# Performance work log

Measured on AMD Instinct MI355X. Metric: run time of the kernel, lower is better.

The kernel has to match this reference:

```python
import jax, jax.numpy as jnp
import numpy as np

B, S, D_IN, D_OUT, N, R = 8, 4096, 1280, 1280, 4, 16


def setup_inputs() -> dict:
    key = jax.random.key(0)
    ks = jax.random.split(key, 7)
    x = jax.random.normal(ks[0], (B, S, D_IN), dtype=jnp.float32)
    W = jax.random.normal(ks[1], (D_OUT, D_IN), dtype=jnp.float32) * 0.02
    bias = jax.random.normal(ks[2], (D_OUT,), dtype=jnp.float32) * 0.02
    A = jax.random.normal(ks[3], (N, R, D_IN), dtype=jnp.float32) * 0.02
    Bw = jax.random.normal(ks[4], (N, D_OUT, R), dtype=jnp.float32) * 0.02
    scalings = jax.random.uniform(ks[5], (N,), dtype=jnp.float32)
    masks = jax.random.uniform(ks[6], (N, S), dtype=jnp.float32)
    # normalize masks to sum ~1 per position, per docstring
    masks = masks / jnp.sum(masks, axis=0, keepdims=True)
    return {"x": x, "W": W, "bias": bias, "A": A, "Bw": Bw,
            "scalings": scalings, "masks": masks}


def reference(x, W, bias, A, Bw, scalings, masks):
    # base linear: y = x @ W^T + b
    base = jnp.einsum('bsd,od->bso', x, W) + bias
    # batched LoRA branches: h = x @ A_i^T  (b,s,n,r)
    h = jnp.einsum('bsd,nrd->bsnr', x, A)
    # lora_out_i = h @ B_i^T  (b,s,n,o)
    lora = jnp.einsum('bsnr,nor->bsno', h, Bw)
    # weighted sum over subjects: scaling_i * mask_i(pos)
    lora_sum = jnp.einsum('bsno,n,ns->bso', lora, scalings, masks)
    return base + lora_sum
```

## Files before the change

kernel.cpp:

```cpp
#include <hip/hip_runtime.h>
#include <hip/hip_bf16.h>
#include <stdint.h>

#define S_LEN   4096
#define DIN     1280
#define DOUT    1280
#define N_LORA  4
#define R_LORA  16
#define M_TOT   32768
#define KC      (DIN + N_LORA*R_LORA)

typedef __attribute__((ext_vector_type(4))) float floatx4;
typedef __attribute__((ext_vector_type(8))) short shortx8;

typedef union { uint4 u; shortx8 s; } punx8;

static __device__ __forceinline__ unsigned short bf16_rne(float f) {
    union { float f; unsigned u; } v; v.f = f;
    unsigned u = v.u;
    u += 0x7fffu + ((u >> 16) & 1u);
    return (unsigned short)(u >> 16);
}

static __device__ __forceinline__ void async16(const unsigned short* g, unsigned short* l) {
    __builtin_amdgcn_global_load_lds(
        (const __attribute__((address_space(1))) unsigned int*)g,
        (__attribute__((address_space(3))) unsigned int*)l, 16, 0, 0);
}

static __device__ __forceinline__ uint4 cvt8(const float* src) {
    const float4* p = (const float4*)src;
    float4 a = p[0], b = p[1];
    uint4 o;
    o.x = (unsigned)bf16_rne(a.x) | ((unsigned)bf16_rne(a.y) << 16);
    o.y = (unsigned)bf16_rne(a.z) | ((unsigned)bf16_rne(a.w) << 16);
    o.z = (unsigned)bf16_rne(b.x) | ((unsigned)bf16_rne(b.y) << 16);
    o.w = (unsigned)bf16_rne(b.z) | ((unsigned)bf16_rne(b.w) << 16);
    return o;
}

__global__ __launch_bounds__(256) void k_build_wcat(const float* __restrict__ W,
                                                    const float* __restrict__ Bw,
                                                    unsigned short* __restrict__ Wcat) {
    int i = blockIdx.x * 256 + threadIdx.x;
    int e = i * 8;
    int o = e / KC;
    int c = e - o * KC;
    const float* src;
    if (c < DIN) {
        src = W + o * DIN + c;
    } else {
        int j = c - DIN;
        int n = j >> 4, r = j & 15;
        src = Bw + (n * DOUT + o) * R_LORA + r;
    }
    *(uint4*)(Wcat + o * KC + c) = cvt8(src);
}

__global__ __launch_bounds__(256) void k_convert_a(const float* __restrict__ A,
                                                   unsigned short* __restrict__ Ab) {
    int i = blockIdx.x * 256 + threadIdx.x;
    int e = i * 8;
    *(uint4*)(Ab + e) = cvt8(A + e);
}

__global__ __launch_bounds__(256) void k_fused_x(const float* __restrict__ x,
                                                 const unsigned short* __restrict__ Ab,
                                                 const float* __restrict__ scalings,
                                                 const float* __restrict__ masks,
                                                 unsigned short* __restrict__ xg) {
    int tid = threadIdx.x;
    int wave = tid >> 6, lane = tid & 63;
    int mi = lane & 15, kq = lane >> 4;
    int m0 = blockIdx.x * 64;
    int m = m0 + wave * 16 + mi;

    const float* xrow = x + (size_t)m * DIN;
    unsigned short* xgrow = xg + (size_t)m * KC;

    floatx4 acc[4] = {};

    for (int k0 = 0; k0 < DIN; k0 += 32) {
        int k = k0 + kq * 8;
        punx8 xf; xf.u = cvt8(xrow + k);
        *(uint4*)(xgrow + k) = xf.u;
#pragma unroll
        for (int ct = 0; ct < 4; ++ct) {
            shortx8 bf = *(const shortx8*)(Ab + (ct * 16 + mi) * DIN + k);
            acc[ct] = __builtin_amdgcn_mfma_f32_16x16x32_bf16(xf.s, bf, acc[ct], 0, 0, 0);
        }
    }

#pragma unroll
    for (int ct = 0; ct < 4; ++ct) {
        float sc = scalings[ct];
        int j = ct * 16 + mi;
#pragma unroll
        for (int reg = 0; reg < 4; ++reg) {
            int m2 = m0 + wave * 16 + kq * 4 + reg;
            int s = m2 & (S_LEN - 1);
            float wgt = sc * masks[ct * S_LEN + s];
            xg[(size_t)m2 * KC + DIN + j] = bf16_rne(acc[ct][reg] * wgt);
        }
    }
}

__global__ __launch_bounds__(256) void k_main_gemm(const unsigned short* __restrict__ xg,
                                                   const unsigned short* __restrict__ Wcat,
                                                   const float* __restrict__ bias,
                                                   float* __restrict__ out) {
    __shared__ unsigned short As[128 * 32];
    __shared__ unsigned short Bs[128 * 32];
    int tid = threadIdx.x;
    int wave = tid >> 6, lane = tid & 63;

    int bx = blockIdx.x;
    int xcd = bx & 7;
    int slot = bx >> 3;
    int rb = xcd * 32 + slot / 10;
    int cb = slot % 10;
    int m0 = rb * 128, n0 = cb * 128;

    int wr = wave >> 1, wc = wave & 1;
    int mi = lane & 15, kq = lane >> 4;

    int c0 = tid, c1 = tid + 256;
    int ar0 = c0 >> 2, ak0 = (c0 & 3) * 8;
    int ar1 = c1 >> 2, ak1 = (c1 & 3) * 8;

    floatx4 acc[4][4] = {};

    for (int k0 = 0; k0 < KC; k0 += 32) {
        async16(xg   + (m0 + ar0) * KC + k0 + ak0, As + c0 * 8);
        async16(xg   + (m0 + ar1) * KC + k0 + ak1, As + c1 * 8);
        async16(Wcat + (n0 + ar0) * KC + k0 + ak0, Bs + c0 * 8);
        async16(Wcat + (n0 + ar1) * KC + k0 + ak1, Bs + c1 * 8);
        __syncthreads();
        shortx8 af[4], bf[4];
#pragma unroll
        for (int t = 0; t < 4; ++t) {
            af[t] = *(const shortx8*)(As + (wr * 64 + t * 16 + mi) * 32 + kq * 8);
            bf[t] = *(const shortx8*)(Bs + (wc * 64 + t * 16 + mi) * 32 + kq * 8);
        }
#pragma unroll
        for (int i = 0; i < 4; ++i)
#pragma unroll
            for (int j = 0; j < 4; ++j)
                acc[i][j] = __builtin_amdgcn_mfma_f32_16x16x32_bf16(af[i], bf[j], acc[i][j], 0, 0, 0);
        __syncthreads();
    }

#pragma unroll
    for (int j = 0; j < 4; ++j) {
        int col = n0 + wc * 64 + j * 16 + mi;
        float bv = bias[col];
#pragma unroll
        for (int i = 0; i < 4; ++i) {
            int rbase = m0 + wr * 64 + i * 16 + kq * 4;
#pragma unroll
            for (int reg = 0; reg < 4; ++reg) {
                out[(size_t)(rbase + reg) * DOUT + col] = acc[i][j][reg] + bv;
            }
        }
    }
}

extern "C" void kernel_launch(void* const* d_in, const int* in_sizes, int n_in,
                              void* d_out, int out_size, void* d_ws, size_t ws_size,
                              hipStream_t stream) {
    const float* x     = (const float*)d_in[0];
    const float* W     = (const float*)d_in[1];
    const float* bias  = (const float*)d_in[2];
    const float* A     = (const float*)d_in[3];
    const float* Bw    = (const float*)d_in[4];
    const float* scal  = (const float*)d_in[5];
    const float* masks = (const float*)d_in[6];
    float* out = (float*)d_out;

    unsigned short* xg   = (unsigned short*)d_ws;
    unsigned short* Wcat = xg + (size_t)M_TOT * KC;
    unsigned short* Ab   = Wcat + (size_t)DOUT * KC;

    k_convert_a<<<(N_LORA * R_LORA * DIN) / (8 * 256), 256, 0, stream>>>(A, Ab);
    k_build_wcat<<<(DOUT * KC) / (8 * 256), 256, 0, stream>>>(W, Bw, Wcat);
    k_fused_x<<<M_TOT / 64, 256, 0, stream>>>(x, Ab, scal, masks, xg);
    k_main_gemm<<<(M_TOT / 128) * (DOUT / 128), 256, 0, stream>>>(xg, Wcat, bias, out);
}
```

Baseline: 474.1 us.

## Split x conversion from LoRA projection and split-K the LoRA down-projection

New measurement: 459.8 us. 3.0% less time.

```diff
diff --git a/kernel.cpp b/kernel.cpp
--- a/kernel.cpp
+++ b/kernel.cpp
@@ -9,6 +9,7 @@
 #define R_LORA  16
 #define M_TOT   32768
 #define KC      (DIN + N_LORA*R_LORA)
+#define NR      64
 
 typedef __attribute__((ext_vector_type(4))) float floatx4;
 typedef __attribute__((ext_vector_type(8))) short shortx8;
@@ -37,6 +38,12 @@
     o.z = (unsigned)bf16_rne(b.x) | ((unsigned)bf16_rne(b.y) << 16);
     o.w = (unsigned)bf16_rne(b.z) | ((unsigned)bf16_rne(b.w) << 16);
     return o;
+}
+
+__global__ __launch_bounds__(256) void k_convert_x(const float* __restrict__ x,
+                                                   unsigned short* __restrict__ xb) {
+    size_t e = ((size_t)blockIdx.x * 256 + threadIdx.x) * 8;
+    *(uint4*)(xb + e) = cvt8(x + e);
 }
 
 __global__ __launch_bounds__(256) void k_build_wcat(const float* __restrict__ W,
@@ -57,55 +64,69 @@
     *(uint4*)(Wcat + o * KC + c) = cvt8(src);
 }
 
-__global__ __launch_bounds__(256) void k_convert_a(const float* __restrict__ A,
-                                                   unsigned short* __restrict__ Ab) {
-    int i = blockIdx.x * 256 + threadIdx.x;
-    int e = i * 8;
-    *(uint4*)(Ab + e) = cvt8(A + e);
-}
-
-__global__ __launch_bounds__(256) void k_fused_x(const float* __restrict__ x,
-                                                 const unsigned short* __restrict__ Ab,
+__global__ __launch_bounds__(256) void k_convert_abp(const float* __restrict__ A,
+                                                     unsigned short* __restrict__ Abp) {
+    int step = blockIdx.x;
+    int t = threadIdx.x;
+    int ct = t >> 6, lane = t & 63;
+    int mi = lane & 15, kq = lane >> 4;
+    const float* src = A + (ct * 16 + mi) * DIN + step * 32 + kq * 8;
+    *(uint4*)(Abp + ((size_t)(step * 4 + ct) * 64 + lane) * 8) = cvt8(src);
+}
+
+__global__ __launch_bounds__(1024) void k_lora_g(const unsigned short* __restrict__ xb,
+                                                 const unsigned short* __restrict__ Abp,
                                                  const float* __restrict__ scalings,
                                                  const float* __restrict__ masks,
-                                                 unsigned short* __restrict__ xg) {
+                                                 unsigned short* __restrict__ g) {
+    __shared__ float hs[4][64][64];
     int tid = threadIdx.x;
     int wave = tid >> 6, lane = tid & 63;
+    int kg = wave >> 2, wv = wave & 3;
     int mi = lane & 15, kq = lane >> 4;
     int m0 = blockIdx.x * 64;
-    int m = m0 + wave * 16 + mi;
-
-    const float* xrow = x + (size_t)m * DIN;
-    unsigned short* xgrow = xg + (size_t)m * KC;
+
+    const unsigned short* xrow = xb + (size_t)(m0 + wv * 16 + mi) * DIN;
 
     floatx4 acc[4] = {};
-
-    for (int k0 = 0; k0 < DIN; k0 += 32) {
-        int k = k0 + kq * 8;
-        punx8 xf; xf.u = cvt8(xrow + k);
-        *(uint4*)(xgrow + k) = xf.u;
+    for (int s = 0; s < 10; ++s) {
+        int step = kg * 10 + s;
+        int k = step * 32 + kq * 8;
+        shortx8 xf = *(const shortx8*)(xrow + k);
 #pragma unroll
         for (int ct = 0; ct < 4; ++ct) {
-            shortx8 bf = *(const shortx8*)(Ab + (ct * 16 + mi) * DIN + k);
-            acc[ct] = __builtin_amdgcn_mfma_f32_16x16x32_bf16(xf.s, bf, acc[ct], 0, 0, 0);
-        }
-    }
-
-#pragma unroll
-    for (int ct = 0; ct < 4; ++ct) {
-        float sc = scalings[ct];
-        int j = ct * 16 + mi;
-#pragma unroll
-        for (int reg = 0; reg < 4; ++reg) {
-            int m2 = m0 + wave * 16 + kq * 4 + reg;
-            int s = m2 & (S_LEN - 1);
-            float wgt = sc * masks[ct * S_LEN + s];
-            xg[(size_t)m2 * KC + DIN + j] = bf16_rne(acc[ct][reg] * wgt);
-        }
-    }
-}
-
-__global__ __launch_bounds__(256) void k_main_gemm(const unsigned short* __restrict__ xg,
+            shortx8 bfr = *(const shortx8*)(Abp + ((size_t)(step * 4 + ct) * 64 + lane) * 8);
+            acc[ct] = __builtin_amdgcn_mfma_f32_16x16x32_bf16(xf, bfr, acc[ct], 0, 0, 0);
+        }
+    }
+#pragma unroll
+    for (int ct = 0; ct < 4; ++ct)
+#pragma unroll
+        for (int reg = 0; reg < 4; ++reg)
+            hs[kg][wv * 16 + kq * 4 + reg][ct * 16 + mi] = acc[ct][reg];
+    __syncthreads();
+
+    int r = tid >> 4;
+    int c0 = (tid & 15) * 4;
+    float4 s0 = *(const float4*)&hs[0][r][c0];
+    float4 s1 = *(const float4*)&hs[1][r][c0];
+    float4 s2 = *(const float4*)&hs[2][r][c0];
+    float4 s3 = *(const float4*)&hs[3][r][c0];
+    int n = c0 >> 4;
+    int m = m0 + r;
+    float wgt = scalings[n] * masks[n * S_LEN + (m & (S_LEN - 1))];
+    float v0 = (s0.x + s1.x + s2.x + s3.x) * wgt;
+    float v1 = (s0.y + s1.y + s2.y + s3.y) * wgt;
+    float v2 = (s0.z + s1.z + s2.z + s3.z) * wgt;
+    float v3 = (s0.w + s1.w + s2.w + s3.w) * wgt;
+    uint2 packed;
+    packed.x = (unsigned)bf16_rne(v0) | ((unsigned)bf16_rne(v1) << 16);
+    packed.y = (unsigned)bf16_rne(v2) | ((unsigned)bf16_rne(v3) << 16);
+    *(uint2*)(g + (size_t)m * NR + c0) = packed;
+}
+
+__global__ __launch_bounds__(256) void k_main_gemm(const unsigned short* __restrict__ xb,
+                                                   const unsigned short* __restrict__ g,
                                                    const unsigned short* __restrict__ Wcat,
                                                    const float* __restrict__ bias,
                                                    float* __restrict__ out) {
@@ -131,10 +152,15 @@
     floatx4 acc[4][4] = {};
 
     for (int k0 = 0; k0 < KC; k0 += 32) {
-        async16(xg   + (m0 + ar0) * KC + k0 + ak0, As + c0 * 8);
-        async16(xg   + (m0 + ar1) * KC + k0 + ak1, As + c1 * 8);
-        async16(Wcat + (n0 + ar0) * KC + k0 + ak0, Bs + c0 * 8);
-        async16(Wcat + (n0 + ar1) * KC + k0 + ak1, Bs + c1 * 8);
+        if (k0 < DIN) {
+            async16(xb + (size_t)(m0 + ar0) * DIN + k0 + ak0, As + c0 * 8);
+            async16(xb + (size_t)(m0 + ar1) * DIN + k0 + ak1, As + c1 * 8);
+        } else {
+            async16(g + (size_t)(m0 + ar0) * NR + (k0 - DIN) + ak0, As + c0 * 8);
+            async16(g + (size_t)(m0 + ar1) * NR + (k0 - DIN) + ak1, As + c1 * 8);
+        }
+        async16(Wcat + (size_t)(n0 + ar0) * KC + k0 + ak0, Bs + c0 * 8);
+        async16(Wcat + (size_t)(n0 + ar1) * KC + k0 + ak1, Bs + c1 * 8);
         __syncthreads();
         shortx8 af[4], bf[4];
 #pragma unroll
@@ -177,12 +203,14 @@
     const float* masks = (const float*)d_in[6];
     float* out = (float*)d_out;
 
-    unsigned short* xg   = (unsigned short*)d_ws;
-    unsigned short* Wcat = xg + (size_t)M_TOT * KC;
-    unsigned short* Ab   = Wcat + (size_t)DOUT * KC;
-
-    k_convert_a<<<(N_LORA * R_LORA * DIN) / (8 * 256), 256, 0, stream>>>(A, Ab);
+    unsigned short* xb   = (unsigned short*)d_ws;
+    unsigned short* g    = xb + (size_t)M_TOT * DIN;
+    unsigned short* Wcat = g + (size_t)M_TOT * NR;
+    unsigned short* Abp  = Wcat + (size_t)DOUT * KC;
+
+    k_convert_x<<<(M_TOT * DIN) / (8 * 256), 256, 0, stream>>>(x, xb);
     k_build_wcat<<<(DOUT * KC) / (8 * 256), 256, 0, stream>>>(W, Bw, Wcat);
-    k_fused_x<<<M_TOT / 64, 256, 0, stream>>>(x, Ab, scal, masks, xg);
-    k_main_gemm<<<(M_TOT / 128) * (DOUT / 128), 256, 0, stream>>>(xg, Wcat, bias, out);
-}
+    k_convert_abp<<<DIN / 32, 256, 0, stream>>>(A, Abp);
+    k_lora_g<<<M_TOT / 64, 1024, 0, stream>>>(xb, Abp, scal, masks, g);
+    k_main_gemm<<<(M_TOT / 128) * (DOUT / 128), 256, 0, stream>>>(xb, g, Wcat, bias, out);
+}
```
